# Kernel tuning notes

Measured on AMD Instinct MI355X. Metric: run time of the kernel, lower is better.

Reference implementation:

```python
import jax, jax.numpy as jnp
import numpy as np

N_NODES = 50000
N_EDGES = 800000
D_IN = 64
D_OUT = 64


def setup_inputs() -> dict:
    key = jax.random.key(0)
    k1, k2, k3 = jax.random.split(key, 3)
    x = jax.random.normal(k1, (N_NODES, D_IN), dtype=jnp.float32)
    edge_index = jax.random.randint(k2, (2, N_EDGES), 0, N_NODES, dtype=jnp.int64)
    # xavier_uniform for weight [in, out]
    limit = np.sqrt(6.0 / (D_IN + D_OUT)).astype(np.float32)
    weight = jax.random.uniform(k3, (D_IN, D_OUT), dtype=jnp.float32, minval=-limit, maxval=limit)
    bias = jnp.zeros((D_OUT,), dtype=jnp.float32)
    return {"x": x, "edge_index": edge_index, "weight": weight, "bias": bias}


def reference(x, edge_index, weight, bias):
    n = x.shape[0]
    # add self loops
    loops = jnp.arange(n, dtype=edge_index.dtype)
    row = jnp.concatenate([edge_index[0], loops])  # [E+N]
    col = jnp.concatenate([edge_index[1], loops])  # [E+N]
    # degree over row (as in torch_geometric degree(row, N))
    deg = jax.ops.segment_sum(jnp.ones_like(row, dtype=x.dtype), row, num_segments=n)
    deg_inv_sqrt = jnp.where(deg > 0, jax.lax.rsqrt(deg), jnp.zeros_like(deg))
    norm = deg_inv_sqrt[row] * deg_inv_sqrt[col]  # [E+N]
    h = x @ weight  # [N, D_OUT]
    # gather-scale-scatter: out[col] += h[row] * norm
    out = jax.ops.segment_sum(h[row] * norm[:, None], col, num_segments=n)
    return out + bias
```

## Files before the change

### kernel.cpp

```cpp
#include <hip/hip_runtime.h>
#include <hip/hip_bf16.h>


constexpr int N_NODES = 50000;
constexpr int N_EDGES = 800000;
constexpr int D = 64;
constexpr int NB_SCAN = (N_NODES + 255) / 256;

constexpr int B_SLICE = 64;
constexpr int SLICE = N_EDGES / B_SLICE;
constexpr int PACK8 = N_NODES / 4;
constexpr int QUAR = N_NODES / 4;
constexpr int NB_GEMM = (N_NODES / 64 + 1 + 3) / 4;

static __device__ __forceinline__ unsigned short f2bf(float f) {
    unsigned u = __float_as_uint(f);
    unsigned r = (u + 0x7fffu + ((u >> 16) & 1u)) >> 16;
    return (unsigned short)r;
}
static __device__ __forceinline__ float bf2f(unsigned short s) {
    return __uint_as_float((unsigned)s << 16);
}

struct GemmLds {
    float Ws[64][64];
    float Xs[4][64][68];
};
constexpr size_t HIST_LDS = (size_t)PACK8 * 4;
constexpr size_t FUSED_LDS = sizeof(GemmLds) > HIST_LDS ? sizeof(GemmLds) : HIST_LDS;

__global__ __launch_bounds__(1024, 4) void fused_hist_gemm(
        const int* __restrict__ ei, unsigned* __restrict__ bh,
        const float* __restrict__ x, const float* __restrict__ W,
        unsigned short* __restrict__ hs) {
    __shared__ __align__(16) char ldsraw[FUSED_LDS];
    const int b = blockIdx.x;
    const int t = threadIdx.x;

    if (b < 2 * B_SLICE) {
        unsigned* loc = (unsigned*)ldsraw;
        int s = b & (B_SLICE - 1);
        const int* arr = (b < B_SLICE) ? ei : ei + N_EDGES;
        for (int w = t; w < PACK8; w += 1024) loc[w] = 0;
        __syncthreads();
        const int* p = arr + s * SLICE;
        for (int i = t; i < SLICE; i += 1024) {
            int k = p[i];
            atomicAdd(&loc[k >> 2], 1u << (8 * (k & 3)));
        }
        __syncthreads();
        unsigned* dst = bh + (size_t)b * PACK8;
        for (int w = t; w < PACK8; w += 1024) dst[w] = loc[w];
    } else {
        GemmLds* g = (GemmLds*)ldsraw;
        const int grp = t >> 8, t256 = t & 255;
        const int tb = (b - 2 * B_SLICE) * 4 + grp;
        const int n0 = tb * 64;

        ((float4*)g->Ws)[t] = ((const float4*)W)[t];

        float (*Xs)[68] = g->Xs[grp];
        const float4* x4 = (const float4*)(x + (size_t)n0 * D);
#pragma unroll
        for (int i = 0; i < 4; ++i) {
            int f = t256 + i * 256;
            int r = f >> 4, c = (f & 15) << 2;
            float4 v = make_float4(0.f, 0.f, 0.f, 0.f);
            if (n0 + r < N_NODES) v = x4[f];
            Xs[r][c] = v.x; Xs[r][c + 1] = v.y; Xs[r][c + 2] = v.z; Xs[r][c + 3] = v.w;
        }
        __syncthreads();

        int tx = t256 & 15, ty = t256 >> 4;
        float acc[4][4] = {};
#pragma unroll 8
        for (int k = 0; k < D; ++k) {
            float a[4], bb[4];
#pragma unroll
            for (int i = 0; i < 4; ++i) a[i] = Xs[ty * 4 + i][k];
#pragma unroll
            for (int jj = 0; jj < 4; ++jj) bb[jj] = g->Ws[k][tx * 4 + jj];
#pragma unroll
            for (int i = 0; i < 4; ++i)
#pragma unroll
                for (int jj = 0; jj < 4; ++jj)
                    acc[i][jj] = fmaf(a[i], bb[jj], acc[i][jj]);
        }

#pragma unroll
        for (int i = 0; i < 4; ++i) {
            int r = ty * 4 + i;
            if (n0 + r < N_NODES) {
                ushort4 v;
                v.x = f2bf(acc[i][0]); v.y = f2bf(acc[i][1]);
                v.z = f2bf(acc[i][2]); v.w = f2bf(acc[i][3]);
                *(ushort4*)(hs + (size_t)(n0 + r) * D + tx * 4) = v;
            }
        }
    }
}

__global__ __launch_bounds__(256) void reduce_scan_kernel(const unsigned* __restrict__ bh,
                                                          float* __restrict__ dis,
                                                          int* __restrict__ offs_local,
                                                          int* __restrict__ partials,
                                                          unsigned char* __restrict__ bs8) {
    int t = threadIdx.x;
    int i = blockIdx.x * 256 + t;
    unsigned cl = 0;
    if (i < N_NODES) {
        const int w = i >> 2;
        const unsigned sh = 8 * (i & 3);
        const unsigned* prow = bh + w;
        unsigned dl = 0;
#pragma unroll
        for (int g = 0; g < 4; ++g) {
            unsigned vr[16];
#pragma unroll
            for (int k = 0; k < 16; ++k) vr[k] = prow[(size_t)(g * 16 + k) * PACK8];
#pragma unroll
            for (int k = 0; k < 16; ++k) dl += (vr[k] >> sh) & 0xffu;
        }
        dis[i] = rsqrtf((float)dl + 1.0f);
        const unsigned* pcol = bh + (size_t)B_SLICE * PACK8 + w;
#pragma unroll
        for (int g = 0; g < 4; ++g) {
            unsigned vr[16];
#pragma unroll
            for (int k = 0; k < 16; ++k) vr[k] = pcol[(size_t)(g * 16 + k) * PACK8];
#pragma unroll
            for (int k = 0; k < 16; ++k) {
                bs8[(size_t)(g * 16 + k) * N_NODES + i] = (unsigned char)cl;
                cl += (vr[k] >> sh) & 0xffu;
            }
        }
    }
    __shared__ int s[256];
    s[t] = (int)cl;
    __syncthreads();
    for (int d = 1; d < 256; d <<= 1) {
        int u = (t >= d) ? s[t - d] : 0;
        __syncthreads();
        s[t] += u;
        __syncthreads();
    }
    if (i < N_NODES) offs_local[i] = s[t] - (int)cl;
    if (t == 255) partials[blockIdx.x] = s[t];
}

__global__ __launch_bounds__(1024) void bucket_det_kernel(const int* __restrict__ ei,
                                                          const int* __restrict__ offs_local,
                                                          const int* __restrict__ partials,
                                                          const unsigned char* __restrict__ bs8,
                                                          int* __restrict__ csr,
                                                          int* __restrict__ offs) {
    __shared__ unsigned pos[QUAR / 4];
    __shared__ int pref[256];
    const int t = threadIdx.x;

    if (t < 256) pref[t] = (t < NB_SCAN) ? partials[t] : 0;
    __syncthreads();
    for (int d = 1; d < 256; d <<= 1) {
        int u = 0;
        if (t < 256 && t >= d) u = pref[t - d];
        __syncthreads();
        if (t < 256) pref[t] += u;
        __syncthreads();
    }
    if (t < 256) {
        int inc = pref[t];
        int own = (t < NB_SCAN) ? partials[t] : 0;
        pref[t] = inc - own;
    }
    __syncthreads();

    const int s = blockIdx.x >> 2;
    const int q = blockIdx.x & 3;
    const int c0 = q * QUAR;

    const unsigned* rel32 = (const unsigned*)(bs8 + (size_t)s * N_NODES + c0);
    for (int w = t; w < QUAR / 4; w += 1024) pos[w] = rel32[w];

    if (s == 0) {
        const int* olq = offs_local + c0;
        for (int w = t; w < QUAR; w += 1024) {
            int node = c0 + w;
            offs[node] = pref[node >> 8] + olq[w];
        }
        if (q == 3 && t == 0) offs[N_NODES] = N_EDGES;
    }
    __syncthreads();

    const int* rowp = ei + s * SLICE;
    const int* colp = ei + N_EDGES + s * SLICE;
    for (int i = t; i < SLICE; i += 1024) {
        int c = colp[i];
        unsigned cc = (unsigned)(c - c0);
        if (cc < (unsigned)QUAR) {
            int base = pref[c >> 8] + offs_local[c];
            unsigned old = atomicAdd(&pos[cc >> 2], 1u << (8 * (cc & 3)));
            unsigned rel = (old >> (8 * (cc & 3))) & 0xffu;
            csr[base + (int)rel] = rowp[i];
        }
    }
}

__global__ __launch_bounds__(256) void gather_kernel(const int* __restrict__ offs,
                                                     const int* __restrict__ csr,
                                                     const unsigned short* __restrict__ hs,
                                                     const float* __restrict__ dis,
                                                     const float* __restrict__ bias,
                                                     float* __restrict__ out) {
    int wave = threadIdx.x >> 6;
    int j = threadIdx.x & 63;
    int n = blockIdx.x * 4 + wave;
    if (n >= N_NODES) return;

    float dn = dis[n];
    float a[8];
    a[0] = dn * bf2f(hs[(size_t)n * D + j]);
#pragma unroll
    for (int k = 1; k < 8; ++k) a[k] = 0.f;

    int beg = __builtin_amdgcn_readfirstlane(offs[n]);
    int m   = __builtin_amdgcn_readfirstlane(offs[n + 1]) - beg;
    const int* p = csr + beg;

    int i = 0;
    for (; i + 16 <= m; i += 16) {
        int r[16];
        float dr[16];
        float v[16];
#pragma unroll
        for (int k = 0; k < 16; ++k) r[k] = p[i + k];
#pragma unroll
        for (int k = 0; k < 16; ++k) dr[k] = dis[r[k]];
#pragma unroll
        for (int k = 0; k < 16; ++k) v[k] = bf2f(hs[(size_t)r[k] * D + j]);
#pragma unroll
        for (int k = 0; k < 16; ++k) a[k & 7] = fmaf(v[k], dr[k], a[k & 7]);
    }
    for (; i + 4 <= m; i += 4) {
        int r0 = p[i], r1 = p[i + 1], r2 = p[i + 2], r3 = p[i + 3];
        a[0] = fmaf(bf2f(hs[(size_t)r0 * D + j]), dis[r0], a[0]);
        a[1] = fmaf(bf2f(hs[(size_t)r1 * D + j]), dis[r1], a[1]);
        a[2] = fmaf(bf2f(hs[(size_t)r2 * D + j]), dis[r2], a[2]);
        a[3] = fmaf(bf2f(hs[(size_t)r3 * D + j]), dis[r3], a[3]);
    }
    for (; i < m; ++i) {
        int r0 = p[i];
        a[1] = fmaf(bf2f(hs[(size_t)r0 * D + j]), dis[r0], a[1]);
    }
    float tot = ((a[0] + a[1]) + (a[2] + a[3])) + ((a[4] + a[5]) + (a[6] + a[7]));
    out[(size_t)n * D + j] = fmaf(dn, tot, bias[j]);
}


__global__ __launch_bounds__(256, 4) void gemm_plain_kernel(const float* __restrict__ x,
                                                            const float* __restrict__ W,
                                                            unsigned short* __restrict__ hs) {
    __shared__ float Xs[64][68];
    __shared__ float Ws[64][64];
    int t = threadIdx.x;
    int n0 = blockIdx.x * 64;

    const float4* W4 = (const float4*)W;
    float4* Ws4 = (float4*)Ws;
#pragma unroll
    for (int i = 0; i < 4; ++i) Ws4[t + i * 256] = W4[t + i * 256];

    const float4* x4 = (const float4*)(x + (size_t)n0 * D);
#pragma unroll
    for (int i = 0; i < 4; ++i) {
        int f = t + i * 256;
        int r = f >> 4, c = (f & 15) << 2;
        float4 v = make_float4(0.f, 0.f, 0.f, 0.f);
        if (n0 + r < N_NODES) v = x4[f];
        Xs[r][c] = v.x; Xs[r][c + 1] = v.y; Xs[r][c + 2] = v.z; Xs[r][c + 3] = v.w;
    }
    __syncthreads();

    int tx = t & 15, ty = t >> 4;
    float acc[4][4] = {};
#pragma unroll 8
    for (int k = 0; k < D; ++k) {
        float a[4], bb[4];
#pragma unroll
        for (int i = 0; i < 4; ++i) a[i] = Xs[ty * 4 + i][k];
#pragma unroll
        for (int jj = 0; jj < 4; ++jj) bb[jj] = Ws[k][tx * 4 + jj];
#pragma unroll
        for (int i = 0; i < 4; ++i)
#pragma unroll
            for (int jj = 0; jj < 4; ++jj)
                acc[i][jj] = fmaf(a[i], bb[jj], acc[i][jj]);
    }

#pragma unroll
    for (int i = 0; i < 4; ++i) {
        int r = ty * 4 + i;
        if (n0 + r < N_NODES) {
            ushort4 v;
            v.x = f2bf(acc[i][0]); v.y = f2bf(acc[i][1]);
            v.z = f2bf(acc[i][2]); v.w = f2bf(acc[i][3]);
            *(ushort4*)(hs + (size_t)(n0 + r) * D + tx * 4) = v;
        }
    }
}

__global__ void histf_kernel(const int* __restrict__ row, const int* __restrict__ col,
                             int* __restrict__ degi, int* __restrict__ cnt) {
    int e = blockIdx.x * blockDim.x + threadIdx.x;
    if (e < N_EDGES) {
        atomicAdd(&degi[row[e]], 1);
        atomicAdd(&cnt[col[e]], 1);
    }
}

__global__ void disf_kernel(int* __restrict__ degi) {
    int i = blockIdx.x * blockDim.x + threadIdx.x;
    if (i < N_NODES) {
        float d = (float)degi[i] + 1.0f;
        ((float*)degi)[i] = rsqrtf(d);
    }
}

__global__ void block_scan_kernel(const int* __restrict__ cnt, int* __restrict__ offs,
                                  int* __restrict__ partials) {
    __shared__ int s[256];
    int t = threadIdx.x;
    int i = blockIdx.x * 256 + t;
    int v = (i < N_NODES) ? cnt[i] : 0;
    s[t] = v;
    __syncthreads();
    for (int d = 1; d < 256; d <<= 1) {
        int u = (t >= d) ? s[t - d] : 0;
        __syncthreads();
        s[t] += u;
        __syncthreads();
    }
    if (i < N_NODES) offs[i] = s[t] - v;
    if (t == 255) partials[blockIdx.x] = s[t];
}

__global__ void scan_partials_kernel(int* __restrict__ partials) {
    __shared__ int s[256];
    int t = threadIdx.x;
    int v = (t < NB_SCAN) ? partials[t] : 0;
    s[t] = v;
    __syncthreads();
    for (int d = 1; d < 256; d <<= 1) {
        int u = (t >= d) ? s[t - d] : 0;
        __syncthreads();
        s[t] += u;
        __syncthreads();
    }
    if (t < NB_SCAN) partials[t] = s[t] - v;
}

__global__ void add_off_kernel(int* __restrict__ offs, const int* __restrict__ partials) {
    int i = blockIdx.x * 256 + threadIdx.x;
    if (i < N_NODES) offs[i] += partials[blockIdx.x];
    if (i == 0) offs[N_NODES] = N_EDGES;
}

__global__ void bucket_fb_kernel(const int* __restrict__ row, const int* __restrict__ col,
                                 const int* __restrict__ offs, int* __restrict__ cur,
                                 int* __restrict__ csr) {
    int e = blockIdx.x * blockDim.x + threadIdx.x;
    if (e < N_EDGES) {
        int c = col[e];
        int pos = offs[c] + atomicAdd(&cur[c], 1);
        csr[pos] = row[e];
    }
}


extern "C" void kernel_launch(void* const* d_in, const int* in_sizes, int n_in,
                              void* d_out, int out_size, void* d_ws, size_t ws_size,
                              hipStream_t stream) {
    const float* x    = (const float*)d_in[0];
    const int*   ei   = (const int*)d_in[1];
    const float* W    = (const float*)d_in[2];
    const float* bias = (const float*)d_in[3];
    float* out = (float*)d_out;

    char* ws = (char*)d_ws;
    float*          dis      = (float*)(ws + 0);
    int*            offs     = (int*)(ws + 200000);
    int*            offs_loc = (int*)(ws + 400064);
    int*            cur      = (int*)(ws + 600064);
    int*            partials = (int*)(ws + 800064);
    int*            csr      = (int*)(ws + 801088);
    unsigned short* hs       = (unsigned short*)(ws + 4001088);
    unsigned*       bh       = (unsigned*)(ws + 10401088);
    unsigned char*  bs8      = (unsigned char*)(ws + 16801088);

    const size_t WS_NEEDED = 20001088;

    if (ws_size >= WS_NEEDED) {
        fused_hist_gemm<<<2 * B_SLICE + NB_GEMM, 1024, 0, stream>>>(ei, bh, x, W, hs);
        reduce_scan_kernel<<<NB_SCAN, 256, 0, stream>>>(bh, dis, offs_loc, partials, bs8);
        bucket_det_kernel<<<4 * B_SLICE, 1024, 0, stream>>>(ei, offs_loc, partials, bs8,
                                                            csr, offs);
        gather_kernel<<<(N_NODES + 3) / 4, 256, 0, stream>>>(offs, csr, hs, dis, bias, out);
    } else {
        const int* row = ei;
        const int* col = ei + N_EDGES;
        int* degi = (int*)dis;
        int* cntf = offs_loc;
        hipMemsetAsync(ws, 0, 800064, stream);
        histf_kernel<<<(N_EDGES + 255) / 256, 256, 0, stream>>>(row, col, degi, cntf);
        disf_kernel<<<(N_NODES + 255) / 256, 256, 0, stream>>>(degi);
        block_scan_kernel<<<NB_SCAN, 256, 0, stream>>>(cntf, offs, partials);
        scan_partials_kernel<<<1, 256, 0, stream>>>(partials);
        add_off_kernel<<<NB_SCAN, 256, 0, stream>>>(offs, partials);
        gemm_plain_kernel<<<(N_NODES + 63) / 64, 256, 0, stream>>>(x, W, hs);
        bucket_fb_kernel<<<(N_EDGES + 255) / 256, 256, 0, stream>>>(row, col, offs, cur, csr);
        gather_kernel<<<(N_NODES + 3) / 4, 256, 0, stream>>>(offs, csr, hs, dis, bias, out);
    }
}
```

Baseline: 135.0 us.

## Move GEMM from histogram kernel into reduce-scan kernel launch

Splits the histogram into its own kernel and instead fuses the x@W GEMM blocks with the reduce/scan blocks in a single 256-thread launch. The GEMM now runs one 64-row tile per 256-thread block rather than four tiles per 1024-thread block. The aim is to keep the long-running histogram blocks, with their large LDS footprint, from being co-scheduled with GEMM work, and to overlap the GEMM with the memory-bound reduce/scan. It changes which work runs concurrently, and the GEMM blocks now occupy the same launch as the scan.

```diff
diff --git a/kernel.cpp b/kernel.cpp
--- a/kernel.cpp
+++ b/kernel.cpp
@@ -11,7 +11,7 @@
 constexpr int SLICE = N_EDGES / B_SLICE;
 constexpr int PACK8 = N_NODES / 4;
 constexpr int QUAR = N_NODES / 4;
-constexpr int NB_GEMM = (N_NODES / 64 + 1 + 3) / 4;
+constexpr int NB_GEMM = (N_NODES + 63) / 64;
 
 static __device__ __forceinline__ unsigned short f2bf(float f) {
     unsigned u = __float_as_uint(f);
@@ -22,64 +22,68 @@
     return __uint_as_float((unsigned)s << 16);
 }
 
-struct GemmLds {
-    float Ws[64][64];
-    float Xs[4][64][68];
-};
-constexpr size_t HIST_LDS = (size_t)PACK8 * 4;
-constexpr size_t FUSED_LDS = sizeof(GemmLds) > HIST_LDS ? sizeof(GemmLds) : HIST_LDS;
-
-__global__ __launch_bounds__(1024, 4) void fused_hist_gemm(
-        const int* __restrict__ ei, unsigned* __restrict__ bh,
+__global__ __launch_bounds__(1024) void hist_priv_kernel(const int* __restrict__ ei,
+                                                         unsigned* __restrict__ bh) {
+    __shared__ unsigned loc[PACK8];
+    int b = blockIdx.x;
+    int s = b & (B_SLICE - 1);
+    const int* arr = (b < B_SLICE) ? ei : ei + N_EDGES;
+    for (int w = threadIdx.x; w < PACK8; w += 1024) loc[w] = 0;
+    __syncthreads();
+    const int* p = arr + s * SLICE;
+    for (int i = threadIdx.x; i < SLICE; i += 1024) {
+        int k = p[i];
+        atomicAdd(&loc[k >> 2], 1u << (8 * (k & 3)));
+    }
+    __syncthreads();
+    unsigned* dst = bh + (size_t)b * PACK8;
+    for (int w = threadIdx.x; w < PACK8; w += 1024) dst[w] = loc[w];
+}
+
+__global__ __launch_bounds__(256, 4) void fused_reduce_gemm(
+        const unsigned* __restrict__ bh,
+        float* __restrict__ dis,
+        int* __restrict__ offs_local,
+        int* __restrict__ partials,
+        unsigned char* __restrict__ bs8,
         const float* __restrict__ x, const float* __restrict__ W,
         unsigned short* __restrict__ hs) {
-    __shared__ __align__(16) char ldsraw[FUSED_LDS];
+    __shared__ union {
+        struct { float Xs[64][68]; float Ws[64][64]; } g;
+        int s[256];
+    } lds;
     const int b = blockIdx.x;
     const int t = threadIdx.x;
 
-    if (b < 2 * B_SLICE) {
-        unsigned* loc = (unsigned*)ldsraw;
-        int s = b & (B_SLICE - 1);
-        const int* arr = (b < B_SLICE) ? ei : ei + N_EDGES;
-        for (int w = t; w < PACK8; w += 1024) loc[w] = 0;
-        __syncthreads();
-        const int* p = arr + s * SLICE;
-        for (int i = t; i < SLICE; i += 1024) {
-            int k = p[i];
-            atomicAdd(&loc[k >> 2], 1u << (8 * (k & 3)));
-        }
-        __syncthreads();
-        unsigned* dst = bh + (size_t)b * PACK8;
-        for (int w = t; w < PACK8; w += 1024) dst[w] = loc[w];
-    } else {
-        GemmLds* g = (GemmLds*)ldsraw;
-        const int grp = t >> 8, t256 = t & 255;
-        const int tb = (b - 2 * B_SLICE) * 4 + grp;
-        const int n0 = tb * 64;
-
-        ((float4*)g->Ws)[t] = ((const float4*)W)[t];
-
-        float (*Xs)[68] = g->Xs[grp];
+    if (b < NB_GEMM) {
+        int n0 = b * 64;
+
+        const float4* W4 = (const float4*)W;
+        float4* Ws4 = (float4*)lds.g.Ws;
+#pragma unroll
+        for (int i = 0; i < 4; ++i) Ws4[t + i * 256] = W4[t + i * 256];
+
         const float4* x4 = (const float4*)(x + (size_t)n0 * D);
 #pragma unroll
         for (int i = 0; i < 4; ++i) {
-            int f = t256 + i * 256;
+            int f = t + i * 256;
             int r = f >> 4, c = (f & 15) << 2;
             float4 v = make_float4(0.f, 0.f, 0.f, 0.f);
             if (n0 + r < N_NODES) v = x4[f];
-            Xs[r][c] = v.x; Xs[r][c + 1] = v.y; Xs[r][c + 2] = v.z; Xs[r][c + 3] = v.w;
-        }
-        __syncthreads();
-
-        int tx = t256 & 15, ty = t256 >> 4;
+            lds.g.Xs[r][c] = v.x; lds.g.Xs[r][c + 1] = v.y;
+            lds.g.Xs[r][c + 2] = v.z; lds.g.Xs[r][c + 3] = v.w;
+        }
+        __syncthreads();
+
+        int tx = t & 15, ty = t >> 4;
         float acc[4][4] = {};
 #pragma unroll 8
         for (int k = 0; k < D; ++k) {
             float a[4], bb[4];
 #pragma unroll
-            for (int i = 0; i < 4; ++i) a[i] = Xs[ty * 4 + i][k];
-#pragma unroll
-            for (int jj = 0; jj < 4; ++jj) bb[jj] = g->Ws[k][tx * 4 + jj];
+            for (int i = 0; i < 4; ++i) a[i] = lds.g.Xs[ty * 4 + i][k];
+#pragma unroll
+            for (int jj = 0; jj < 4; ++jj) bb[jj] = lds.g.Ws[k][tx * 4 + jj];
 #pragma unroll
             for (int i = 0; i < 4; ++i)
 #pragma unroll
@@ -97,55 +101,48 @@
                 *(ushort4*)(hs + (size_t)(n0 + r) * D + tx * 4) = v;
             }
         }
-    }
-}
-
-__global__ __launch_bounds__(256) void reduce_scan_kernel(const unsigned* __restrict__ bh,
-                                                          float* __restrict__ dis,
-                                                          int* __restrict__ offs_local,
-                                                          int* __restrict__ partials,
-                                                          unsigned char* __restrict__ bs8) {
-    int t = threadIdx.x;
-    int i = blockIdx.x * 256 + t;
-    unsigned cl = 0;
-    if (i < N_NODES) {
-        const int w = i >> 2;
-        const unsigned sh = 8 * (i & 3);
-        const unsigned* prow = bh + w;
-        unsigned dl = 0;
-#pragma unroll
-        for (int g = 0; g < 4; ++g) {
-            unsigned vr[16];
-#pragma unroll
-            for (int k = 0; k < 16; ++k) vr[k] = prow[(size_t)(g * 16 + k) * PACK8];
-#pragma unroll
-            for (int k = 0; k < 16; ++k) dl += (vr[k] >> sh) & 0xffu;
-        }
-        dis[i] = rsqrtf((float)dl + 1.0f);
-        const unsigned* pcol = bh + (size_t)B_SLICE * PACK8 + w;
-#pragma unroll
-        for (int g = 0; g < 4; ++g) {
-            unsigned vr[16];
-#pragma unroll
-            for (int k = 0; k < 16; ++k) vr[k] = pcol[(size_t)(g * 16 + k) * PACK8];
-#pragma unroll
-            for (int k = 0; k < 16; ++k) {
-                bs8[(size_t)(g * 16 + k) * N_NODES + i] = (unsigned char)cl;
-                cl += (vr[k] >> sh) & 0xffu;
+    } else {
+        const int rb = b - NB_GEMM;
+        int i = rb * 256 + t;
+        unsigned cl = 0;
+        if (i < N_NODES) {
+            const int w = i >> 2;
+            const unsigned sh = 8 * (i & 3);
+            const unsigned* prow = bh + w;
+            unsigned dl = 0;
+#pragma unroll
+            for (int g = 0; g < 4; ++g) {
+                unsigned vr[16];
+#pragma unroll
+                for (int k = 0; k < 16; ++k) vr[k] = prow[(size_t)(g * 16 + k) * PACK8];
+#pragma unroll
+                for (int k = 0; k < 16; ++k) dl += (vr[k] >> sh) & 0xffu;
             }
-        }
-    }
-    __shared__ int s[256];
-    s[t] = (int)cl;
-    __syncthreads();
-    for (int d = 1; d < 256; d <<= 1) {
-        int u = (t >= d) ? s[t - d] : 0;
-        __syncthreads();
-        s[t] += u;
-        __syncthreads();
-    }
-    if (i < N_NODES) offs_local[i] = s[t] - (int)cl;
-    if (t == 255) partials[blockIdx.x] = s[t];
+            dis[i] = rsqrtf((float)dl + 1.0f);
+            const unsigned* pcol = bh + (size_t)B_SLICE * PACK8 + w;
+#pragma unroll
+            for (int g = 0; g < 4; ++g) {
+                unsigned vr[16];
+#pragma unroll
+                for (int k = 0; k < 16; ++k) vr[k] = pcol[(size_t)(g * 16 + k) * PACK8];
+#pragma unroll
+                for (int k = 0; k < 16; ++k) {
+                    bs8[(size_t)(g * 16 + k) * N_NODES + i] = (unsigned char)cl;
+                    cl += (vr[k] >> sh) & 0xffu;
+                }
+            }
+        }
+        lds.s[t] = (int)cl;
+        __syncthreads();
+        for (int d = 1; d < 256; d <<= 1) {
+            int u = (t >= d) ? lds.s[t - d] : 0;
+            __syncthreads();
+            lds.s[t] += u;
+            __syncthreads();
+        }
+        if (i < N_NODES) offs_local[i] = lds.s[t] - (int)cl;
+        if (t == 255) partials[rb] = lds.s[t];
+    }
 }
 
 __global__ __launch_bounds__(1024) void bucket_det_kernel(const int* __restrict__ ei,
@@ -399,8 +396,9 @@
     const size_t WS_NEEDED = 20001088;
 
     if (ws_size >= WS_NEEDED) {
-        fused_hist_gemm<<<2 * B_SLICE + NB_GEMM, 1024, 0, stream>>>(ei, bh, x, W, hs);
-        reduce_scan_kernel<<<NB_SCAN, 256, 0, stream>>>(bh, dis, offs_loc, partials, bs8);
+        hist_priv_kernel<<<2 * B_SLICE, 1024, 0, stream>>>(ei, bh);
+        fused_reduce_gemm<<<NB_GEMM + NB_SCAN, 256, 0, stream>>>(bh, dis, offs_loc,
+                                                                 partials, bs8, x, W, hs);
         bucket_det_kernel<<<4 * B_SLICE, 1024, 0, stream>>>(ei, offs_loc, partials, bs8,
                                                             csr, offs);
         gather_kernel<<<(N_NODES + 3) / 4, 256, 0, stream>>>(offs, csr, hs, dis, bias, out);
```

Result: no change. 135.9 us (+0.6%).
